# Kernel optimization log

Hardware: AMD Instinct MI355X
Metric: run time of the kernel (lower is better)

Reference implementation:

```python
import jax, jax.numpy as jnp
import numpy as np

N, M, B, C, L, H = 8192, 8192, 16, 512, 64, 8
HEAD_DIM = C // H
PER_BATCH_KEYS = M // B
MASK_VAL = -1000.0  # matches torch masked_fill_ value


def setup_inputs() -> dict:
    key0 = jax.random.key(0)
    ks = jax.random.split(key0, 8)
    query = jax.random.normal(ks[0], (N, C), jnp.float32)
    key = jax.random.normal(ks[1], (M, C), jnp.float32)
    value = jax.random.normal(ks[2], (M, C), jnp.float32)
    # xavier-ish init for projections
    in_proj_weight = jax.random.normal(ks[3], (3 * C, C), jnp.float32) * (1.0 / np.sqrt(C))
    in_proj_bias = jnp.zeros((3 * C,), jnp.float32)
    out_w = jax.random.normal(ks[4], (C, C), jnp.float32) * (1.0 / np.sqrt(C))
    out_b = jnp.zeros((C,), jnp.float32)
    index_pair = jax.random.randint(ks[5], (N, L), 0, PER_BATCH_KEYS).astype(jnp.int32)
    pad = jax.random.uniform(ks[6], (N, L)) < 0.05
    index_pair = jnp.where(pad, jnp.int32(-1), index_pair)
    query_batch_cnt = jnp.full((B,), N // B, jnp.int32)
    key_batch_cnt = jnp.full((B,), PER_BATCH_KEYS, jnp.int32)
    index_pair_batch = jnp.repeat(jnp.arange(B, dtype=jnp.int32), N // B)
    return {
        "query": query, "key": key, "value": value,
        "in_proj_weight": in_proj_weight, "in_proj_bias": in_proj_bias,
        "out_w": out_w, "out_b": out_b,
        "index_pair": index_pair, "query_batch_cnt": query_batch_cnt,
        "key_batch_cnt": key_batch_cnt, "index_pair_batch": index_pair_batch,
    }


def reference(query, key, value, in_proj_weight, in_proj_bias, out_w, out_b,
              index_pair, query_batch_cnt, key_batch_cnt, index_pair_batch):
    embed_dim = query.shape[-1]
    scaling = float(HEAD_DIM) ** -0.5
    # qkv projections (in_proj_weight is [3C, C], applied as F.linear => x @ W.T + b)
    q = (query @ in_proj_weight[:embed_dim].T + in_proj_bias[:embed_dim]) * scaling
    k = key @ in_proj_weight[embed_dim:2 * embed_dim].T + in_proj_bias[embed_dim:2 * embed_dim]
    v = value @ in_proj_weight[2 * embed_dim:].T + in_proj_bias[2 * embed_dim:]
    q = q.reshape(N, H, HEAD_DIM)
    k = k.reshape(M, H, HEAD_DIM)
    v = v.reshape(M, H, HEAD_DIM)
    # local -> global key indices: offset by start of each query's batch key block
    key_start = jnp.cumsum(key_batch_cnt) - key_batch_cnt          # (B,)
    offset = key_start[index_pair_batch]                            # (N,)
    valid = index_pair >= 0                                         # (N, L)
    gidx = jnp.where(valid, index_pair + offset[:, None], 0)        # (N, L), safe gather
    # gather-based scores: (N, L, H)
    scores = jnp.einsum("nhd,nlhd->nlh", q, k[gidx])
    scores = jnp.where(valid[..., None], scores, MASK_VAL)
    w = jax.nn.softmax(scores, axis=1)                              # softmax over neighbors L
    # weighted value sum; masked weights underflow to exactly 0 in fp32
    attn = jnp.einsum("nlh,nlhd->nhd", w, v[gidx]).reshape(N, embed_dim)
    attn = attn @ out_w.T + out_b
    return attn, w.sum(axis=-1) / H
```

## Files before the change

kernel.cpp:

```cpp
#include <hip/hip_runtime.h>
#include <hip/hip_bf16.h>
#include <math.h>

#define NQ 8192
#define MK 8192
#define CD 512
#define LN 64
#define HH 8
#define HD 64
#define BB 16

typedef short short8 __attribute__((ext_vector_type(8)));
typedef float floatx4 __attribute__((ext_vector_type(4)));

__device__ __forceinline__ unsigned short f2bf(float x) {
    unsigned int u = __builtin_bit_cast(unsigned int, x);
    return (unsigned short)((u + 0x7FFFu + ((u >> 16) & 1u)) >> 16);
}
__device__ __forceinline__ unsigned int pkbf(float lo, float hi) {
    float2 f; f.x = lo; f.y = hi;
    __hip_bfloat162 h2 = __float22bfloat162_rn(f);
    unsigned int u;
    __builtin_memcpy(&u, &h2, 4);
    return u;
}
__device__ __forceinline__ float bflo(unsigned int u) {
    return __builtin_bit_cast(float, u << 16);
}
__device__ __forceinline__ float bfhij(unsigned int u) {
    return __builtin_bit_cast(float, u);
}
__device__ __forceinline__ short8 u4s8(uint4 u) {
    short8 s; __builtin_memcpy(&s, &u, 16); return s;
}

__device__ __forceinline__ void gl_lds16(const unsigned short* g, unsigned short* l) {
    __builtin_amdgcn_global_load_lds(
        (const __attribute__((address_space(1))) unsigned int*)g,
        (__attribute__((address_space(3))) unsigned int*)l, 16, 0, 0);
}

struct ConvSeg { const float* src; unsigned short* dst; int n4; };
struct ConvArgs { ConvSeg s[5]; };

__global__ __launch_bounds__(256) void convert_bf16(ConvArgs a) {
    const int seg = blockIdx.y;
    const int i = blockIdx.x * 256 + threadIdx.x;
    if (i >= a.s[seg].n4) return;
    const float4 v = ((const float4*)a.s[seg].src)[i];
    uint2 o; o.x = pkbf(v.x, v.y); o.y = pkbf(v.z, v.w);
    ((uint2*)a.s[seg].dst)[i] = o;
}

__device__ __forceinline__ void gemm_bf_body(const unsigned short* __restrict__ A,
                                             const unsigned short* __restrict__ W,
                                             const float* __restrict__ bias,
                                             float* __restrict__ outf,
                                             unsigned short* __restrict__ outb,
                                             float scale) {
    __shared__ unsigned short As[128 * 64];
    __shared__ unsigned short Bs[128 * 64];

    const int tid  = threadIdx.x;
    const int row0 = blockIdx.x * 128;
    const int col0 = blockIdx.y * 128;

    const int w    = tid >> 6;
    const int lane = tid & 63;
    const int wr   = w >> 1;
    const int wc   = w & 1;
    const int q    = lane >> 4;
    const int ml   = lane & 15;

    const int sr = lane >> 3;
    const int sg = (lane & 7) ^ sr;
    const unsigned short* Ap = A + (size_t)(row0 + w * 32 + sr) * CD + sg * 8;
    const unsigned short* Wp = W + (size_t)(col0 + w * 32 + sr) * CD + sg * 8;
    unsigned short* Asw = &As[(w * 32) * 64];
    unsigned short* Bsw = &Bs[(w * 32) * 64];

    floatx4 acc[4][4];
#pragma unroll
    for (int i = 0; i < 4; ++i)
#pragma unroll
        for (int j = 0; j < 4; ++j)
            acc[i][j] = (floatx4){0.f, 0.f, 0.f, 0.f};

    for (int k0 = 0; k0 < CD; k0 += 64) {
        __syncthreads();
#pragma unroll
        for (int i = 0; i < 4; ++i) {
            gl_lds16(Ap + (size_t)(i * 8) * CD + k0, Asw + i * 8 * 64);
            gl_lds16(Wp + (size_t)(i * 8) * CD + k0, Bsw + i * 8 * 64);
        }
        __syncthreads();

#pragma unroll
        for (int kw = 0; kw < 2; ++kw) {
            short8 af[4], bf[4];
            const int gp = ((kw * 4 + q) ^ (ml & 7)) * 8;
#pragma unroll
            for (int mi = 0; mi < 4; ++mi)
                af[mi] = *(const short8*)&As[(wr * 64 + mi * 16 + ml) * 64 + gp];
#pragma unroll
            for (int ni = 0; ni < 4; ++ni)
                bf[ni] = *(const short8*)&Bs[(wc * 64 + ni * 16 + ml) * 64 + gp];
#pragma unroll
            for (int mi = 0; mi < 4; ++mi)
#pragma unroll
                for (int ni = 0; ni < 4; ++ni)
                    acc[mi][ni] = __builtin_amdgcn_mfma_f32_16x16x32_bf16(
                        af[mi], bf[ni], acc[mi][ni], 0, 0, 0);
        }
    }

    float bv[4];
#pragma unroll
    for (int ni = 0; ni < 4; ++ni)
        bv[ni] = bias[col0 + wc * 64 + ni * 16 + ml];
#pragma unroll
    for (int mi = 0; mi < 4; ++mi) {
#pragma unroll
        for (int ni = 0; ni < 4; ++ni) {
            const int cg = col0 + wc * 64 + ni * 16 + ml;
#pragma unroll
            for (int r = 0; r < 4; ++r) {
                const int rg = row0 + wr * 64 + mi * 16 + q * 4 + r;
                const float val = (acc[mi][ni][r] + bv[ni]) * scale;
                if (outb) outb[(size_t)rg * CD + cg] = f2bf(val);
                else      outf[(size_t)rg * CD + cg] = val;
            }
        }
    }
}

__global__ __launch_bounds__(256) void qkv_gemm(const unsigned short* __restrict__ A_bf,
                                                const unsigned short* __restrict__ w_bf,
                                                const float* __restrict__ bias,
                                                unsigned short* __restrict__ q_bf,
                                                unsigned short* __restrict__ k_bf,
                                                unsigned short* __restrict__ v_bf) {
    const int z = blockIdx.z;
    const unsigned short* A = A_bf + (size_t)z * NQ * CD;
    unsigned short* outb = (z == 0) ? q_bf : ((z == 1) ? k_bf : v_bf);
    gemm_bf_body(A, w_bf + (size_t)z * CD * CD, bias + (size_t)z * CD,
                 nullptr, outb, (z == 0) ? 0.125f : 1.0f);
}

__global__ __launch_bounds__(256) void out_gemm(const unsigned short* __restrict__ A,
                                                const unsigned short* __restrict__ W,
                                                const float* __restrict__ bias,
                                                float* __restrict__ out) {
    gemm_bf_body(A, W, bias, out, nullptr, 1.0f);
}

__global__ __launch_bounds__(512) void attn_kernel(
    const unsigned short* __restrict__ q_bf,
    const unsigned short* __restrict__ k_bf,
    const unsigned short* __restrict__ v_bf,
    const int* __restrict__ index_pair,
    const int* __restrict__ key_batch_cnt,
    const int* __restrict__ index_pair_batch,
    unsigned short* __restrict__ attn_bf,
    float* __restrict__ out2) {
    const int j = blockIdx.x;
    const int n = (j & 7) * (NQ / 8) + (j >> 3);

    const int tid  = threadIdx.x;
    const int h    = tid >> 6;
    const int lane = tid & 63;
    const int quad = lane >> 4;
    const int ml   = lane & 15;

    __shared__ float wmat[HH][LN];
    __shared__ int   gs[LN];

    if (tid < LN) {
        const int batch = index_pair_batch[n];
        int offset = 0;
        for (int b = 0; b < batch; ++b) offset += key_batch_cnt[b];
        const int gi = index_pair[n * LN + tid];
        gs[tid] = (gi >= 0) ? (gi + offset) : 0;
    }
    __syncthreads();

    const char* qp = (const char*)q_bf + (size_t)n * (CD * 2) + h * (HD * 2) + quad * 16;
    const short8 bq0 = u4s8(*(const uint4*)qp);
    const short8 bq1 = u4s8(*(const uint4*)(qp + 64));

    int gr[4];
#pragma unroll
    for (int g = 0; g < 4; ++g) gr[g] = gs[g * 16 + ml];
    uint4 a0[4], a1[4];
#pragma unroll
    for (int g = 0; g < 4; ++g) {
        const char* kp = (const char*)k_bf + (size_t)gr[g] * (CD * 2) + h * (HD * 2) + quad * 16;
        a0[g] = *(const uint4*)kp;
        a1[g] = *(const uint4*)(kp + 64);
    }
#pragma unroll
    for (int g = 0; g < 4; ++g) {
        floatx4 sa = (floatx4){0.f, 0.f, 0.f, 0.f};
        sa = __builtin_amdgcn_mfma_f32_16x16x32_bf16(u4s8(a0[g]), bq0, sa, 0, 0, 0);
        sa = __builtin_amdgcn_mfma_f32_16x16x32_bf16(u4s8(a1[g]), bq1, sa, 0, 0, 0);
        if (ml == 0) {
#pragma unroll
            for (int r = 0; r < 4; ++r) wmat[h][g * 16 + quad * 4 + r] = sa[r];
        }
    }

    float score = wmat[h][lane];
    if (index_pair[n * LN + lane] < 0) score = -1000.0f;
    float mx = score;
#pragma unroll
    for (int o = 32; o > 0; o >>= 1) mx = fmaxf(mx, __shfl_xor(mx, o, 64));
    float e = __expf(score - mx);
    float s = e;
#pragma unroll
    for (int o = 32; o > 0; o >>= 1) s += __shfl_xor(s, o, 64);
    const float w = e / s;
    wmat[h][lane] = w;
    __syncthreads();

    const int r  = lane >> 3;
    const int dg = lane & 7;
    unsigned int off[8];
#pragma unroll
    for (int it = 0; it < 8; ++it)
        off[it] = (unsigned int)gs[it * 8 + r] * (CD * 2) + h * (HD * 2) + dg * 16;

    float a8[8] = {0.f, 0.f, 0.f, 0.f, 0.f, 0.f, 0.f, 0.f};
#pragma unroll
    for (int it = 0; it < 8; ++it) {
        const float wl = __shfl(w, it * 8 + r, 64);
        const uint4 vv = *(const uint4*)((const char*)v_bf + off[it]);
        a8[0] = fmaf(wl, bflo(vv.x),  a8[0]);
        a8[1] = fmaf(wl, bfhij(vv.x), a8[1]);
        a8[2] = fmaf(wl, bflo(vv.y),  a8[2]);
        a8[3] = fmaf(wl, bfhij(vv.y), a8[3]);
        a8[4] = fmaf(wl, bflo(vv.z),  a8[4]);
        a8[5] = fmaf(wl, bfhij(vv.z), a8[5]);
        a8[6] = fmaf(wl, bflo(vv.w),  a8[6]);
        a8[7] = fmaf(wl, bfhij(vv.w), a8[7]);
    }
#pragma unroll
    for (int o = 8; o <= 32; o <<= 1)
#pragma unroll
        for (int d = 0; d < 8; ++d) a8[d] += __shfl_xor(a8[d], o, 64);
    attn_bf[(size_t)n * CD + h * HD + dg * 8 + r] = f2bf(a8[r]);

    if (tid < LN) {
        float s8 = 0.f;
#pragma unroll
        for (int hh = 0; hh < HH; ++hh) s8 += wmat[hh][tid];
        out2[(size_t)n * LN + tid] = s8 * (1.0f / HH);
    }
}

extern "C" void kernel_launch(void* const* d_in, const int* in_sizes, int n_in,
                              void* d_out, int out_size, void* d_ws, size_t ws_size,
                              hipStream_t stream) {
    const float* query   = (const float*)d_in[0];
    const float* key     = (const float*)d_in[1];
    const float* value   = (const float*)d_in[2];
    const float* ipw     = (const float*)d_in[3];
    const float* ipb     = (const float*)d_in[4];
    const float* out_w   = (const float*)d_in[5];
    const float* out_b   = (const float*)d_in[6];
    const int*   index_pair       = (const int*)d_in[7];
    const int*   key_batch_cnt    = (const int*)d_in[9];
    const int*   index_pair_batch = (const int*)d_in[10];

    float* out = (float*)d_out;
    unsigned short* q_bf  = (unsigned short*)d_ws;
    unsigned short* k_bf  = q_bf + (size_t)NQ * CD;
    unsigned short* v_bf  = k_bf + (size_t)NQ * CD;
    unsigned short* A_bf  = v_bf + (size_t)NQ * CD;
    unsigned short* w_bf  = A_bf + (size_t)3 * NQ * CD;
    unsigned short* ow_bf = w_bf + (size_t)3 * CD * CD;
    unsigned short* attn_bf = A_bf;

    ConvArgs ca;
    ca.s[0] = {query, A_bf,                       NQ * CD / 4};
    ca.s[1] = {key,   A_bf + (size_t)NQ * CD,     NQ * CD / 4};
    ca.s[2] = {value, A_bf + (size_t)2 * NQ * CD, NQ * CD / 4};
    ca.s[3] = {ipw,   w_bf,                       3 * CD * CD / 4};
    ca.s[4] = {out_w, ow_bf,                      CD * CD / 4};
    dim3 g0(NQ * CD / 4 / 256, 5);
    convert_bf16<<<g0, 256, 0, stream>>>(ca);

    dim3 g1(NQ / 128, CD / 128, 3);
    qkv_gemm<<<g1, 256, 0, stream>>>(A_bf, w_bf, ipb, q_bf, k_bf, v_bf);

    attn_kernel<<<NQ, 512, 0, stream>>>(q_bf, k_bf, v_bf, index_pair,
                                        key_batch_cnt, index_pair_batch,
                                        attn_bf, out + (size_t)NQ * CD);

    dim3 g3(NQ / 128, CD / 128, 1);
    out_gemm<<<g3, 256, 0, stream>>>(attn_bf, ow_bf, out_b, out);
}
```

Baseline: 233.2 us.

## Prefetch V gather before score MFMA and replace serial batch offset scan

```diff
diff --git a/kernel.cpp b/kernel.cpp
--- a/kernel.cpp
+++ b/kernel.cpp
@@ -154,7 +154,7 @@
     gemm_bf_body(A, W, bias, out, nullptr, 1.0f);
 }
 
-__global__ __launch_bounds__(512) void attn_kernel(
+__global__ __launch_bounds__(512, 4) void attn_kernel(
     const unsigned short* __restrict__ q_bf,
     const unsigned short* __restrict__ k_bf,
     const unsigned short* __restrict__ v_bf,
@@ -174,13 +174,22 @@
 
     __shared__ float wmat[HH][LN];
     __shared__ int   gs[LN];
+    __shared__ unsigned long long smask;
 
     if (tid < LN) {
+        int incl = (lane < BB) ? key_batch_cnt[lane] : 0;
+#pragma unroll
+        for (int d = 1; d < BB; d <<= 1) {
+            const int t = __shfl_up(incl, d, 64);
+            if (lane >= d) incl += t;
+        }
         const int batch = index_pair_batch[n];
-        int offset = 0;
-        for (int b = 0; b < batch; ++b) offset += key_batch_cnt[b];
-        const int gi = index_pair[n * LN + tid];
-        gs[tid] = (gi >= 0) ? (gi + offset) : 0;
+        int off0 = 0;
+        if (batch > 0) off0 = __shfl(incl, batch - 1, 64);
+        const int gi = index_pair[n * LN + lane];
+        const unsigned long long vm = __ballot(gi >= 0);
+        if (lane == 0) smask = vm;
+        gs[lane] = (gi >= 0) ? (gi + off0) : 0;
     }
     __syncthreads();
 
@@ -198,6 +207,16 @@
         a0[g] = *(const uint4*)kp;
         a1[g] = *(const uint4*)(kp + 64);
     }
+    const int r  = lane >> 3;
+    const int dg = lane & 7;
+    uint4 vv[8];
+#pragma unroll
+    for (int it = 0; it < 8; ++it) {
+        const unsigned int off = (unsigned int)gs[it * 8 + r] * (CD * 2)
+                                 + h * (HD * 2) + dg * 16;
+        vv[it] = *(const uint4*)((const char*)v_bf + off);
+    }
+
 #pragma unroll
     for (int g = 0; g < 4; ++g) {
         floatx4 sa = (floatx4){0.f, 0.f, 0.f, 0.f};
@@ -205,12 +224,12 @@
         sa = __builtin_amdgcn_mfma_f32_16x16x32_bf16(u4s8(a1[g]), bq1, sa, 0, 0, 0);
         if (ml == 0) {
 #pragma unroll
-            for (int r = 0; r < 4; ++r) wmat[h][g * 16 + quad * 4 + r] = sa[r];
+            for (int rr = 0; rr < 4; ++rr) wmat[h][g * 16 + quad * 4 + rr] = sa[rr];
         }
     }
 
     float score = wmat[h][lane];
-    if (index_pair[n * LN + lane] < 0) score = -1000.0f;
+    if (!((smask >> lane) & 1ull)) score = -1000.0f;
     float mx = score;
 #pragma unroll
     for (int o = 32; o > 0; o >>= 1) mx = fmaxf(mx, __shfl_xor(mx, o, 64));
@@ -220,28 +239,19 @@
     for (int o = 32; o > 0; o >>= 1) s += __shfl_xor(s, o, 64);
     const float w = e / s;
     wmat[h][lane] = w;
-    __syncthreads();
-
-    const int r  = lane >> 3;
-    const int dg = lane & 7;
-    unsigned int off[8];
-#pragma unroll
-    for (int it = 0; it < 8; ++it)
-        off[it] = (unsigned int)gs[it * 8 + r] * (CD * 2) + h * (HD * 2) + dg * 16;
 
     float a8[8] = {0.f, 0.f, 0.f, 0.f, 0.f, 0.f, 0.f, 0.f};
 #pragma unroll
     for (int it = 0; it < 8; ++it) {
         const float wl = __shfl(w, it * 8 + r, 64);
-        const uint4 vv = *(const uint4*)((const char*)v_bf + off[it]);
-        a8[0] = fmaf(wl, bflo(vv.x),  a8[0]);
-        a8[1] = fmaf(wl, bfhij(vv.x), a8[1]);
-        a8[2] = fmaf(wl, bflo(vv.y),  a8[2]);
-        a8[3] = fmaf(wl, bfhij(vv.y), a8[3]);
-        a8[4] = fmaf(wl, bflo(vv.z),  a8[4]);
-        a8[5] = fmaf(wl, bfhij(vv.z), a8[5]);
-        a8[6] = fmaf(wl, bflo(vv.w),  a8[6]);
-        a8[7] = fmaf(wl, bfhij(vv.w), a8[7]);
+        a8[0] = fmaf(wl, bflo(vv[it].x),  a8[0]);
+        a8[1] = fmaf(wl, bfhij(vv[it].x), a8[1]);
+        a8[2] = fmaf(wl, bflo(vv[it].y),  a8[2]);
+        a8[3] = fmaf(wl, bfhij(vv[it].y), a8[3]);
+        a8[4] = fmaf(wl, bflo(vv[it].z),  a8[4]);
+        a8[5] = fmaf(wl, bfhij(vv[it].z), a8[5]);
+        a8[6] = fmaf(wl, bflo(vv[it].w),  a8[6]);
+        a8[7] = fmaf(wl, bfhij(vv[it].w), a8[7]);
     }
 #pragma unroll
     for (int o = 8; o <= 32; o <<= 1)
@@ -249,6 +259,7 @@
         for (int d = 0; d < 8; ++d) a8[d] += __shfl_xor(a8[d], o, 64);
     attn_bf[(size_t)n * CD + h * HD + dg * 8 + r] = f2bf(a8[r]);
 
+    __syncthreads();
     if (tid < LN) {
         float s8 = 0.f;
 #pragma unroll
```

After: 223.7 us. -4.1%, faster.
